# Optimization experiments

Hardware: AMD Instinct MI355X
Metric: run time of the kernel (lower is better)

## Reference

```python
import jax, jax.numpy as jnp
import numpy as np

B, T = 2, 2048
D_MODEL = 1024
N_LAYERS = 2
VOCAB = 256
BLOCK = 2048
LOCAL = 128
STRIDE = 256
NHEAD = D_MODEL // 64  # 16
HEAD_DIM = D_MODEL // NHEAD  # 64
LN_EPS = 1e-5


def setup_inputs() -> dict:
    key = jax.random.key(0)
    ks = jax.random.split(key, 16)
    L, d = N_LAYERS, D_MODEL

    def g(k, shape, scale=0.02):
        return (jax.random.normal(k, shape, dtype=jnp.float32) * scale)

    return {
        "x": jax.random.randint(ks[0], (B, T), 0, VOCAB),
        "embed": g(ks[1], (VOCAB, d)),
        "pos_embed": g(ks[2], (BLOCK, d)),
        # per-layer weights stacked on leading L axis; Linear as y = x @ W + b
        "Wq": g(ks[3], (L, d, d)), "bq": jnp.zeros((L, d), jnp.float32),
        "Wk": g(ks[4], (L, d, d)), "bk": jnp.zeros((L, d), jnp.float32),
        "Wv": g(ks[5], (L, d, d)), "bv": jnp.zeros((L, d), jnp.float32),
        "Wo": g(ks[6], (L, d, d)), "bo": jnp.zeros((L, d), jnp.float32),
        "g1": jnp.ones((L, d), jnp.float32), "be1": jnp.zeros((L, d), jnp.float32),
        "W1": g(ks[7], (L, d, 4 * d)), "bf1": jnp.zeros((L, 4 * d), jnp.float32),
        "W2": g(ks[8], (L, 4 * d, d)), "bf2": jnp.zeros((L, d), jnp.float32),
        "g2": jnp.ones((L, d), jnp.float32), "be2": jnp.zeros((L, d), jnp.float32),
        "gf": jnp.ones((d,), jnp.float32), "bef": jnp.zeros((d,), jnp.float32),
        "Whead": g(ks[9], (d, VOCAB)),
    }


def _ln(x, gamma, beta):
    mu = jnp.mean(x, axis=-1, keepdims=True)
    var = jnp.mean(jnp.square(x - mu), axis=-1, keepdims=True)
    return (x - mu) * jax.lax.rsqrt(var + LN_EPS) * gamma + beta


def _sparse_mask(t):
    # allowed[i, j] = True if token i may attend to token j
    i = jnp.arange(t)[:, None]
    j = jnp.arange(t)[None, :]
    causal = j <= i
    local = (i - j) <= LOCAL
    glob = (j % STRIDE) == 0
    return causal & (local | glob)


def _sparse_attn(q, k, v, allowed):
    # q, k, v: [B, T, D] -> [B, H, T, hd]
    b, t, d = q.shape
    def split(x):
        return x.reshape(b, t, NHEAD, HEAD_DIM).transpose(0, 2, 1, 3)
    q, k, v = split(q), split(k), split(v)
    scale = HEAD_DIM ** -0.5
    scores = jnp.einsum("bhqd,bhkd->bhqk", q, k) * scale
    scores = jnp.where(allowed[None, None], scores, -jnp.inf)
    attn = jax.nn.softmax(scores, axis=-1)  # every row has j=i allowed -> no NaN
    out = jnp.einsum("bhqk,bhkd->bhqd", attn, v)
    return out.transpose(0, 2, 1, 3).reshape(b, t, d)


def reference(x, embed, pos_embed, Wq, bq, Wk, bk, Wv, bv, Wo, bo,
              g1, be1, W1, bf1, W2, bf2, g2, be2, gf, bef, Whead):
    b, t = x.shape
    h = embed[x] + pos_embed[jnp.arange(t)][None]
    allowed = _sparse_mask(t)
    for l in range(N_LAYERS):
        h_n = _ln(h, g1[l], be1[l])
        q = h_n @ Wq[l] + bq[l]
        k = h_n @ Wk[l] + bk[l]
        v = h_n @ Wv[l] + bv[l]
        attn_out = _sparse_attn(q, k, v, allowed)
        h = h + (attn_out @ Wo[l] + bo[l])
        h2 = _ln(h, g2[l], be2[l])
        ffn = jax.nn.gelu(h2 @ W1[l] + bf1[l], approximate=False) @ W2[l] + bf2[l]
        h = h + ffn
    h = _ln(h, gf, bef)
    return h @ Whead
```

## Files before the change

### kernel.cpp

```cpp
#include <hip/hip_runtime.h>
#include <hip/hip_bf16.h>

#define BB 2
#define TT 2048
#define DD 1024
#define FF 4096
#define VV 256
#define HH 16
#define HD 64
#define MM (BB * TT)
#define LOCAL_W 128
#define STRIDE_G 256
#define QS 3072

typedef short s16x8 __attribute__((ext_vector_type(8)));
typedef __bf16 bf16x8 __attribute__((ext_vector_type(8)));
typedef float f32x4 __attribute__((ext_vector_type(4)));

#define WAITVM(N) asm volatile("s_waitcnt vmcnt(" #N ")" ::: "memory")
#define LGKM0 do { asm volatile("s_waitcnt lgkmcnt(0)" ::: "memory"); \
                   __builtin_amdgcn_sched_barrier(0); } while (0)

__device__ __forceinline__ float b2f(unsigned short u) {
  return __builtin_bit_cast(float, (unsigned int)u << 16);
}
__device__ __forceinline__ unsigned short f2b(float f) {
  __hip_bfloat16 h = __float2bfloat16(f);
  return __builtin_bit_cast(unsigned short, h);
}
__device__ __forceinline__ void gl_lds16(const unsigned short* g, unsigned short* l) {
  __builtin_amdgcn_global_load_lds(
      (const __attribute__((address_space(1))) void*)g,
      (__attribute__((address_space(3))) void*)l, 16, 0, 0);
}
__device__ __forceinline__ bf16x8 ldsr(const unsigned short* p) {
  return __builtin_bit_cast(bf16x8, *(const s16x8*)p);
}

__global__ __launch_bounds__(256) void transpose_k(const float* __restrict__ W,
                                                   unsigned short* __restrict__ WT,
                                                   int K, int N) {
  __shared__ float t[32][33];
  const int n0 = blockIdx.x * 32, k0 = blockIdx.y * 32;
  const int tx = threadIdx.x, ty = threadIdx.y;
  for (int r = ty; r < 32; r += 8) t[r][tx] = W[(size_t)(k0 + r) * N + n0 + tx];
  __syncthreads();
  for (int r = ty; r < 32; r += 8)
    WT[(size_t)(n0 + r) * K + k0 + tx] = f2b(t[tx][r]);
}

__global__ __launch_bounds__(256) void concat_bias(const float* __restrict__ bq,
                                                   const float* __restrict__ bk,
                                                   const float* __restrict__ bv,
                                                   float* __restrict__ bcat) {
  const int i = blockIdx.x * 256 + threadIdx.x;
  const int l = i / QS, j = i - l * QS;
  float v;
  if (j < DD) v = bq[l * DD + j];
  else if (j < 2 * DD) v = bk[l * DD + j - DD];
  else v = bv[l * DD + j - 2 * DD];
  bcat[i] = v;
}

__global__ __launch_bounds__(256) void embed_kernel(const int* __restrict__ x,
                                                    const float* __restrict__ emb,
                                                    const float* __restrict__ pos,
                                                    float* __restrict__ h) {
  const int row = blockIdx.x;
  const int c = threadIdx.x * 4;
  const int tok = x[row];
  const int t = row & (TT - 1);
  float4 e = *(const float4*)&emb[(size_t)tok * DD + c];
  float4 p = *(const float4*)&pos[(size_t)t * DD + c];
  e.x += p.x; e.y += p.y; e.z += p.z; e.w += p.w;
  *(float4*)&h[(size_t)row * DD + c] = e;
}

__global__ __launch_bounds__(256) void ln_kernel(const float* __restrict__ x,
                                                 const float* __restrict__ g,
                                                 const float* __restrict__ be,
                                                 unsigned short* __restrict__ out) {
  const int row = blockIdx.x;
  const int tid = threadIdx.x;
  const float4 v = *(const float4*)&x[(size_t)row * DD + tid * 4];
  float s = v.x + v.y + v.z + v.w;
  float sq = v.x * v.x + v.y * v.y + v.z * v.z + v.w * v.w;
#pragma unroll
  for (int off = 32; off; off >>= 1) {
    s += __shfl_xor(s, off);
    sq += __shfl_xor(sq, off);
  }
  __shared__ float ss[4], ssq[4];
  const int w = tid >> 6, lane = tid & 63;
  if (lane == 0) { ss[w] = s; ssq[w] = sq; }
  __syncthreads();
  s = ss[0] + ss[1] + ss[2] + ss[3];
  sq = ssq[0] + ssq[1] + ssq[2] + ssq[3];
  const float mean = s * (1.0f / DD);
  const float var = sq * (1.0f / DD) - mean * mean;
  const float rstd = rsqrtf(var + 1e-5f);
  const float4 gv = *(const float4*)&g[tid * 4];
  const float4 bv = *(const float4*)&be[tid * 4];
  ushort4 o;
  o.x = f2b((v.x - mean) * rstd * gv.x + bv.x);
  o.y = f2b((v.y - mean) * rstd * gv.y + bv.y);
  o.z = f2b((v.z - mean) * rstd * gv.z + bv.z);
  o.w = f2b((v.w - mean) * rstd * gv.w + bv.w);
  *(ushort4*)&out[(size_t)row * DD + tid * 4] = o;
}

template <int EPI>
__global__ __launch_bounds__(512, 2) void gemm8p(const unsigned short* __restrict__ A,
                                                 const unsigned short* __restrict__ BT,
                                                 const float* __restrict__ bias,
                                                 unsigned short* __restrict__ outp,
                                                 int M, int N, int K, int nbx) {
  __shared__ __align__(16) unsigned short lds[65536];
  const int tid = threadIdx.x;
  const int lane = tid & 63;
  const int w = tid >> 6;
  const int nwg = gridDim.x;
  const int orig = blockIdx.x;
  const int wg = (orig & 7) * (nwg >> 3) + (orig >> 3);
  const int n0 = (wg % nbx) * 256, m0 = (wg / nbx) * 256;
  const int wm = w >> 2, wn = w & 3;
  f32x4 acc[8][4] = {};

  const unsigned short* aSrc[2];
  const unsigned short* bSrc[2];
  int dstO[2];
#pragma unroll
  for (int i = 0; i < 2; i++) {
    const int s = tid + (i << 9);
    const int row = s >> 2, sc = s & 3;
    const int l = sc ^ ((row >> 1) & 3);
    aSrc[i] = &A[(size_t)(m0 + row) * K + l * 8];
    bSrc[i] = &BT[(size_t)(n0 + row) * K + l * 8];
    dstO[i] = s * 8;
  }
  auto STAGE = [&](int tb, int ks, int obase) {
    const int kt = (tb << 6) + (ks << 5);
    const int so = obase + ks * 16384;
#pragma unroll
    for (int i = 0; i < 2; i++) {
      gl_lds16(aSrc[i] + kt, &lds[so + dstO[i]]);
      gl_lds16(bSrc[i] + kt, &lds[so + 8192 + dstO[i]]);
    }
  };

  const int rA = lane & 15, cr = lane >> 4;
  const int rowA0 = wm * 128 + rA;
  const int rowB0 = wn * 64 + rA;
  const int aAddr0 = rowA0 * 32 + ((cr ^ ((rowA0 >> 1) & 3)) << 3);
  const int bAddr0 = 8192 + rowB0 * 32 + ((cr ^ ((rowB0 >> 1) & 3)) << 3);

  const int NT = K >> 6;
  STAGE(0, 0, 0);
  STAGE(0, 1, 0);

  auto TILE = [&](int bufc, int tb, bool notlast) {
    const int bb = bufc << 15;
    const int ob = (bufc ^ 1) << 15;
    bf16x8 bfr[4], af[4];
    WAITVM(4);
    __builtin_amdgcn_s_barrier();
#pragma unroll
    for (int n = 0; n < 4; n++) bfr[n] = ldsr(&lds[bb + bAddr0 + n * 512]);
#pragma unroll
    for (int i = 0; i < 4; i++) af[i] = ldsr(&lds[bb + aAddr0 + i * 512]);
    if (notlast) STAGE(tb + 1, 0, ob);
    LGKM0;
    __builtin_amdgcn_s_setprio(1);
#pragma unroll
    for (int i = 0; i < 4; i++)
#pragma unroll
      for (int n = 0; n < 4; n++)
        acc[i][n] = __builtin_amdgcn_mfma_f32_16x16x32_bf16(af[i], bfr[n], acc[i][n], 0, 0, 0);
    __builtin_amdgcn_s_setprio(0);
#pragma unroll
    for (int i = 0; i < 4; i++) af[i] = ldsr(&lds[bb + aAddr0 + (4 + i) * 512]);
    LGKM0;
    __builtin_amdgcn_s_setprio(1);
#pragma unroll
    for (int i = 0; i < 4; i++)
#pragma unroll
      for (int n = 0; n < 4; n++)
        acc[4 + i][n] = __builtin_amdgcn_mfma_f32_16x16x32_bf16(af[i], bfr[n], acc[4 + i][n], 0, 0, 0);
    __builtin_amdgcn_s_setprio(0);
    if (notlast) { WAITVM(4); } else { WAITVM(0); }
    __builtin_amdgcn_s_barrier();
#pragma unroll
    for (int n = 0; n < 4; n++) bfr[n] = ldsr(&lds[bb + 16384 + bAddr0 + n * 512]);
#pragma unroll
    for (int i = 0; i < 4; i++) af[i] = ldsr(&lds[bb + 16384 + aAddr0 + i * 512]);
    if (notlast) STAGE(tb + 1, 1, ob);
    LGKM0;
    __builtin_amdgcn_s_setprio(1);
#pragma unroll
    for (int i = 0; i < 4; i++)
#pragma unroll
      for (int n = 0; n < 4; n++)
        acc[i][n] = __builtin_amdgcn_mfma_f32_16x16x32_bf16(af[i], bfr[n], acc[i][n], 0, 0, 0);
    __builtin_amdgcn_s_setprio(0);
#pragma unroll
    for (int i = 0; i < 4; i++) af[i] = ldsr(&lds[bb + 16384 + aAddr0 + (4 + i) * 512]);
    LGKM0;
    __builtin_amdgcn_s_setprio(1);
#pragma unroll
    for (int i = 0; i < 4; i++)
#pragma unroll
      for (int n = 0; n < 4; n++)
        acc[4 + i][n] = __builtin_amdgcn_mfma_f32_16x16x32_bf16(af[i], bfr[n], acc[4 + i][n], 0, 0, 0);
    __builtin_amdgcn_s_setprio(0);
  };

  for (int it = 0; it < NT; it += 2) {
    TILE(0, it, true);
    TILE(1, it + 1, it + 2 < NT);
  }

  const int r0 = (lane >> 4) * 4;
  const int cc = lane & 15;
#pragma unroll
  for (int m = 0; m < 8; m++) {
#pragma unroll
    for (int n = 0; n < 4; n++) {
#pragma unroll
      for (int r = 0; r < 4; r++) {
        const int row = m0 + wm * 128 + m * 16 + r0 + r;
        const int col = n0 + wn * 64 + n * 16 + cc;
        float val = acc[m][n][r] + bias[col];
        if (EPI == 3) {
          float u = val * (0.7978845608f + 0.0356774081f * val * val);
          u = fminf(u, 10.0f);
          const float e = __expf(2.0f * u);
          val = val * e / (e + 1.0f);
        }
        outp[(size_t)row * N + col] = f2b(val);
      }
    }
  }
}

template <int EPI>
__global__ __launch_bounds__(512, 2) void gemm_p(const unsigned short* __restrict__ A,
                                                 const unsigned short* __restrict__ BT,
                                                 const float* __restrict__ bias,
                                                 const float* __restrict__ res,
                                                 void* __restrict__ outp,
                                                 int M, int N, int K, int nbx, int nwg2,
                                                 int ksub) {
  constexpr int BM = 128;
  __shared__ __align__(16) unsigned short lds[4][BM * 64];
  const int tid = threadIdx.x;
  const int lane = tid & 63;
  const int w = tid >> 6;
  const int nwg = gridDim.x;
  const int orig = blockIdx.x;
  const int wg = (orig & 7) * (nwg >> 3) + (orig >> 3);
  const int ks = wg / nwg2;
  const int rem = wg - ks * nwg2;
  const int n0 = (rem % nbx) * BM;
  const int m0 = (rem / nbx) * BM;
  const int kb = ks * ksub;
  const int wm = w >> 2, wn = w & 3;
  f32x4 acc[4][2] = {};

  auto STAGE = [&](int t) {
    const int b = t & 3;
    const int kt = kb + (t << 5);
    const int s = tid;
    const int row = s >> 2, sc = s & 3;
    const int c = sc ^ ((row >> 1) & 3);
    gl_lds16(&A[(size_t)(m0 + row) * K + kt + c * 8], &lds[b][s * 8]);
    gl_lds16(&BT[(size_t)(n0 + row) * K + kt + c * 8], &lds[b][BM * 32 + s * 8]);
  };

  const int NT = ksub >> 5;
  STAGE(0); STAGE(1); STAGE(2);

  for (int t = 0; t < NT; ++t) {
    const int ahead = NT - 1 - t;
    if (ahead >= 2) WAITVM(4); else if (ahead == 1) WAITVM(2); else WAITVM(0);
    __builtin_amdgcn_s_barrier();
    asm volatile("" ::: "memory");
    if (t + 3 < NT) STAGE(t + 3);
    const int b = t & 3;
    const int rA = lane & 15, cr = lane >> 4;
    bf16x8 af[4], bfr[2];
#pragma unroll
    for (int m = 0; m < 4; m++) {
      const int row = wm * 64 + m * 16 + rA;
      af[m] = ldsr(&lds[b][row * 32 + ((cr ^ ((row >> 1) & 3)) << 3)]);
    }
#pragma unroll
    for (int n = 0; n < 2; n++) {
      const int row = wn * 32 + n * 16 + rA;
      bfr[n] = ldsr(&lds[b][BM * 32 + row * 32 + ((cr ^ ((row >> 1) & 3)) << 3)]);
    }
    __builtin_amdgcn_s_setprio(1);
#pragma unroll
    for (int m = 0; m < 4; m++)
#pragma unroll
      for (int n = 0; n < 2; n++)
        acc[m][n] = __builtin_amdgcn_mfma_f32_16x16x32_bf16(af[m], bfr[n], acc[m][n], 0, 0, 0);
    __builtin_amdgcn_s_setprio(0);
  }

  const int r0 = (lane >> 4) * 4;
  const int cc = lane & 15;
  float* pout = (EPI == 0) ? ((float*)outp + (size_t)ks * M * N) : (float*)outp;
#pragma unroll
  for (int m = 0; m < 4; m++) {
#pragma unroll
    for (int n = 0; n < 2; n++) {
#pragma unroll
      for (int r = 0; r < 4; r++) {
        const int row = m0 + wm * 64 + m * 16 + r0 + r;
        const int col = n0 + wn * 32 + n * 16 + cc;
        const size_t idx = (size_t)row * N + col;
        if (EPI == 0) {
          pout[idx] = acc[m][n][r];
        } else {
          ((float*)outp)[idx] = acc[m][n][r] + bias[col] + res[idx];
        }
      }
    }
  }
}

template <int NP, bool BIAS, bool RES>
__global__ __launch_bounds__(256) void reduce_k(float* __restrict__ dst,
                                                const float* __restrict__ parts,
                                                const float* __restrict__ bias,
                                                int ncols, size_t total) {
  const size_t i = ((size_t)blockIdx.x * 256 + threadIdx.x) * 4;
  if (i >= total) return;
  f32x4 acc = {};
  if (RES) acc = *(const f32x4*)&dst[i];
  if (BIAS) {
    const int col = (int)(i % ncols);
    acc += *(const f32x4*)&bias[col];
  }
#pragma unroll
  for (int p = 0; p < NP; p++) acc += *(const f32x4*)&parts[(size_t)p * total + i];
  *(f32x4*)&dst[i] = acc;
}

#define QT 16
#define KT 32
#define NTMAX 6
#define KP 72
#define PP 40

__global__ __launch_bounds__(256) void attn_mfma(const unsigned short* __restrict__ qkv,
                                                 unsigned short* __restrict__ outg) {
  __shared__ __align__(16) unsigned short kvs[4][KT * KP];
  __shared__ __align__(16) unsigned short pls[4][QT * PP];
  const int tid = threadIdx.x;
  const int wid = tid >> 6, lane = tid & 63;
  const int qgrp = blockIdx.x & 31;
  const int bh = blockIdx.x >> 5;
  const int h = bh & (HH - 1), b = bh >> 4;
  const size_t baseq = (size_t)b * TT * QS + (size_t)h * HD;
  const size_t baseo = (size_t)b * TT * DD + (size_t)h * HD;
  const int i0 = qgrp * 64 + wid * 16;
  const int g = lane >> 4;
  const int c = lane & 15;

  const int i0b = qgrp * 64 + 48;
  const int ka0b = (i0b > 128) ? ((i0b - 128) & ~31) : 0;
  const int nlb = ((i0b + 16 - ka0b) + 31) >> 5;
  const int neb = (ka0b + 255) >> 8;
  const int ka0 = (i0 > 128) ? ((i0 - 128) & ~31) : 0;
  const int ne = (ka0 + 255) >> 8;

  const s16x8 qf0 = *(const s16x8*)&qkv[baseq + (size_t)(i0 + c) * QS + g * 8];
  const s16x8 qf1 = *(const s16x8*)&qkv[baseq + (size_t)(i0 + c) * QS + 32 + g * 8];

  f32x4 sc[NTMAX][2];
  float smax[4] = {-1e30f, -1e30f, -1e30f, -1e30f};

#pragma unroll
  for (int t = 0; t < NTMAX; t++) {
    if (t > nlb) continue;
    const bool isg = (t == 0);
    if (isg && neb == 0) continue;
    const int kt0 = ka0 + (t - 1) * 32;
#pragma unroll
    for (int it = 0; it < 4; it++) {
      const int row = it * 8 + (lane >> 3);
      const int ch = lane & 7;
      const int j = isg ? ((row < ne) ? row * STRIDE_G : 0) : (kt0 + row);
      *(s16x8*)&kvs[wid][row * KP + ch * 8] =
          *(const s16x8*)&qkv[baseq + DD + (size_t)j * QS + ch * 8];
    }
    __syncthreads();
#pragma unroll
    for (int half = 0; half < 2; half++) {
      const int key = half * 16 + c;
      const bf16x8 kb0 = __builtin_bit_cast(bf16x8, *(const s16x8*)&kvs[wid][key * KP + g * 8]);
      const bf16x8 kb1 = __builtin_bit_cast(bf16x8, *(const s16x8*)&kvs[wid][key * KP + 32 + g * 8]);
      f32x4 a = {};
      a = __builtin_amdgcn_mfma_f32_16x16x32_bf16(__builtin_bit_cast(bf16x8, qf0), kb0, a, 0, 0, 0);
      a = __builtin_amdgcn_mfma_f32_16x16x32_bf16(__builtin_bit_cast(bf16x8, qf1), kb1, a, 0, 0, 0);
#pragma unroll
      for (int r = 0; r < 4; r++) {
        const int i = i0 + g * 4 + r;
        bool ok;
        if (isg) {
          ok = (key < ne);
        } else {
          const int j = kt0 + key;
          ok = (j <= i) && (((i - j) <= LOCAL_W) || ((j & (STRIDE_G - 1)) == 0));
        }
        const float s = ok ? a[r] * 0.125f : -1e30f;
        sc[t][half][r] = s;
        smax[r] = fmaxf(smax[r], s);
      }
    }
    __syncthreads();
  }
#pragma unroll
  for (int r = 0; r < 4; r++)
#pragma unroll
    for (int off = 8; off; off >>= 1)
      smax[r] = fmaxf(smax[r], __shfl_xor(smax[r], off));

  f32x4 o[4] = {};
  float lsum[4] = {0.f, 0.f, 0.f, 0.f};
#pragma unroll
  for (int t = 0; t < NTMAX; t++) {
    if (t > nlb) continue;
    const bool isg = (t == 0);
    if (isg && neb == 0) continue;
    const int kt0 = ka0 + (t - 1) * 32;
#pragma unroll
    for (int it = 0; it < 4; it++) {
      const int row = it * 8 + (lane >> 3);
      const int ch = lane & 7;
      const int j = isg ? ((row < ne) ? row * STRIDE_G : 0) : (kt0 + row);
      *(s16x8*)&kvs[wid][row * KP + ch * 8] =
          *(const s16x8*)&qkv[baseq + 2 * DD + (size_t)j * QS + ch * 8];
    }
#pragma unroll
    for (int half = 0; half < 2; half++)
#pragma unroll
      for (int r = 0; r < 4; r++) {
        const float p = __expf(sc[t][half][r] - smax[r]);
        lsum[r] += p;
        pls[wid][(g * 4 + r) * PP + half * 16 + c] = f2b(p);
      }
    __syncthreads();
    const bf16x8 pa = __builtin_bit_cast(bf16x8, *(const s16x8*)&pls[wid][c * PP + g * 8]);
#pragma unroll
    for (int d0 = 0; d0 < 4; d0++) {
      s16x8 bv;
#pragma unroll
      for (int e = 0; e < 8; e++)
        bv[e] = (short)kvs[wid][(g * 8 + e) * KP + d0 * 16 + c];
      o[d0] = __builtin_amdgcn_mfma_f32_16x16x32_bf16(pa, __builtin_bit_cast(bf16x8, bv), o[d0], 0, 0, 0);
    }
    __syncthreads();
  }
#pragma unroll
  for (int r = 0; r < 4; r++)
#pragma unroll
    for (int off = 8; off; off >>= 1)
      lsum[r] += __shfl_xor(lsum[r], off);
#pragma unroll
  for (int d0 = 0; d0 < 4; d0++)
#pragma unroll
    for (int r = 0; r < 4; r++)
      outg[baseo + (size_t)(i0 + g * 4 + r) * DD + d0 * 16 + c] = f2b(o[d0][r] / lsum[r]);
}

extern "C" void kernel_launch(void* const* d_in, const int* in_sizes, int n_in,
                              void* d_out, int out_size, void* d_ws, size_t ws_size,
                              hipStream_t stream) {
  const int* x = (const int*)d_in[0];
  const float* embed = (const float*)d_in[1];
  const float* pos = (const float*)d_in[2];
  const float* Wq = (const float*)d_in[3];
  const float* bq = (const float*)d_in[4];
  const float* Wk = (const float*)d_in[5];
  const float* bk = (const float*)d_in[6];
  const float* Wv = (const float*)d_in[7];
  const float* bv = (const float*)d_in[8];
  const float* Wo = (const float*)d_in[9];
  const float* bo = (const float*)d_in[10];
  const float* g1 = (const float*)d_in[11];
  const float* be1 = (const float*)d_in[12];
  const float* W1 = (const float*)d_in[13];
  const float* bf1 = (const float*)d_in[14];
  const float* W2 = (const float*)d_in[15];
  const float* bf2 = (const float*)d_in[16];
  const float* g2 = (const float*)d_in[17];
  const float* be2 = (const float*)d_in[18];
  const float* gf = (const float*)d_in[19];
  const float* bef = (const float*)d_in[20];
  const float* Whead = (const float*)d_in[21];

  char* ws = (char*)d_ws;
  size_t off = 0;
  auto alloc = [&](size_t bytes) -> void* {
    void* p = ws + off;
    off += (bytes + 255) & ~(size_t)255;
    return p;
  };
  unsigned short* WqkvT = (unsigned short*)alloc((size_t)2 * QS * DD * 2);
  unsigned short* WoT = (unsigned short*)alloc((size_t)2 * DD * DD * 2);
  unsigned short* W1T = (unsigned short*)alloc((size_t)2 * DD * FF * 2);
  unsigned short* W2T = (unsigned short*)alloc((size_t)2 * DD * FF * 2);
  unsigned short* WheadT = (unsigned short*)alloc((size_t)DD * VV * 2);
  float* bcat = (float*)alloc((size_t)2 * QS * 4);
  float* h = (float*)alloc((size_t)MM * DD * 4);
  unsigned short* hn = (unsigned short*)alloc((size_t)MM * DD * 2);
  unsigned short* qkvb = (unsigned short*)alloc((size_t)MM * QS * 2);
  unsigned short* attnb = (unsigned short*)alloc((size_t)MM * DD * 2);
  unsigned short* mid = (unsigned short*)alloc((size_t)MM * FF * 2);
  float* ffn2p = (float*)qkvb;
  float* headp = (float*)mid;
  (void)ws_size;

  const dim3 tb(32, 8);
  for (int l = 0; l < 2; l++) {
    const size_t wo = (size_t)l * DD * DD;
    const size_t wf = (size_t)l * DD * FF;
    transpose_k<<<dim3(DD / 32, DD / 32), tb, 0, stream>>>(Wq + wo, WqkvT + (size_t)l * QS * DD, DD, DD);
    transpose_k<<<dim3(DD / 32, DD / 32), tb, 0, stream>>>(Wk + wo, WqkvT + ((size_t)l * QS + DD) * DD, DD, DD);
    transpose_k<<<dim3(DD / 32, DD / 32), tb, 0, stream>>>(Wv + wo, WqkvT + ((size_t)l * QS + 2 * DD) * DD, DD, DD);
    transpose_k<<<dim3(DD / 32, DD / 32), tb, 0, stream>>>(Wo + wo, WoT + wo, DD, DD);
    transpose_k<<<dim3(FF / 32, DD / 32), tb, 0, stream>>>(W1 + wf, W1T + wf, DD, FF);
    transpose_k<<<dim3(DD / 32, FF / 32), tb, 0, stream>>>(W2 + wf, W2T + wf, FF, DD);
  }
  transpose_k<<<dim3(VV / 32, DD / 32), tb, 0, stream>>>(Whead, WheadT, DD, VV);
  concat_bias<<<24, 256, 0, stream>>>(bq, bk, bv, bcat);

  embed_kernel<<<MM, 256, 0, stream>>>(x, embed, pos, h);

  for (int l = 0; l < 2; l++) {
    const size_t wo = (size_t)l * DD * DD;
    const size_t wf = (size_t)l * DD * FF;
    ln_kernel<<<MM, 256, 0, stream>>>(h, g1 + l * DD, be1 + l * DD, hn);
    gemm8p<1><<<(QS / 256) * (MM / 256), 512, 0, stream>>>(
        hn, WqkvT + (size_t)l * QS * DD, bcat + l * QS, qkvb, MM, QS, DD, QS / 256);
    attn_mfma<<<BB * HH * (TT / 64), 256, 0, stream>>>(qkvb, attnb);
    gemm_p<2><<<(DD / 128) * (MM / 128), 512, 0, stream>>>(
        attnb, WoT + wo, bo + l * DD, h, h,
        MM, DD, DD, DD / 128, (DD / 128) * (MM / 128), DD);
    ln_kernel<<<MM, 256, 0, stream>>>(h, g2 + l * DD, be2 + l * DD, hn);
    gemm8p<3><<<(FF / 256) * (MM / 256), 512, 0, stream>>>(
        hn, W1T + wf, bf1 + l * FF, mid, MM, FF, DD, FF / 256);
    gemm_p<0><<<2 * (DD / 128) * (MM / 128), 512, 0, stream>>>(
        mid, W2T + wf, nullptr, nullptr, ffn2p,
        MM, DD, FF, DD / 128, (DD / 128) * (MM / 128), FF / 2);
    reduce_k<2, true, true><<<(MM * DD) / 1024, 256, 0, stream>>>(
        h, ffn2p, bf2 + l * DD, DD, (size_t)MM * DD);
  }
  ln_kernel<<<MM, 256, 0, stream>>>(h, gf, bef, hn);
  gemm_p<0><<<4 * (VV / 128) * (MM / 128), 512, 0, stream>>>(
      hn, WheadT, nullptr, nullptr, headp,
      MM, VV, DD, VV / 128, (VV / 128) * (MM / 128), DD / 4);
  reduce_k<4, false, false><<<(MM * VV) / 1024, 256, 0, stream>>>(
      (float*)d_out, headp, nullptr, VV, (size_t)MM * VV);
}
```

Before: 455.9 us.

## Fuse FFN split-K reduction with next LayerNorm and add 256x128 W2 GEMM

Result: faster. 438.6 us (-3.8%).

```diff
diff --git a/kernel.cpp b/kernel.cpp
--- a/kernel.cpp
+++ b/kernel.cpp
@@ -109,6 +109,46 @@
   *(ushort4*)&out[(size_t)row * DD + tid * 4] = o;
 }
 
+__global__ __launch_bounds__(256) void ln_red(float* __restrict__ hio,
+                                              const float* __restrict__ parts,
+                                              const float* __restrict__ bias,
+                                              const float* __restrict__ g,
+                                              const float* __restrict__ be,
+                                              unsigned short* __restrict__ out) {
+  const int row = blockIdx.x;
+  const int tid = threadIdx.x;
+  const size_t base = (size_t)row * DD + tid * 4;
+  f32x4 v = *(const f32x4*)&hio[base];
+  v += *(const f32x4*)&bias[tid * 4];
+  v += *(const f32x4*)&parts[base];
+  v += *(const f32x4*)&parts[(size_t)MM * DD + base];
+  *(f32x4*)&hio[base] = v;
+  float s = v[0] + v[1] + v[2] + v[3];
+  float sq = v[0] * v[0] + v[1] * v[1] + v[2] * v[2] + v[3] * v[3];
+#pragma unroll
+  for (int off = 32; off; off >>= 1) {
+    s += __shfl_xor(s, off);
+    sq += __shfl_xor(sq, off);
+  }
+  __shared__ float ss[4], ssq[4];
+  const int w = tid >> 6, lane = tid & 63;
+  if (lane == 0) { ss[w] = s; ssq[w] = sq; }
+  __syncthreads();
+  s = ss[0] + ss[1] + ss[2] + ss[3];
+  sq = ssq[0] + ssq[1] + ssq[2] + ssq[3];
+  const float mean = s * (1.0f / DD);
+  const float var = sq * (1.0f / DD) - mean * mean;
+  const float rstd = rsqrtf(var + 1e-5f);
+  const float4 gv = *(const float4*)&g[tid * 4];
+  const float4 bv = *(const float4*)&be[tid * 4];
+  ushort4 o;
+  o.x = f2b((v[0] - mean) * rstd * gv.x + bv.x);
+  o.y = f2b((v[1] - mean) * rstd * gv.y + bv.y);
+  o.z = f2b((v[2] - mean) * rstd * gv.z + bv.z);
+  o.w = f2b((v[3] - mean) * rstd * gv.w + bv.w);
+  *(ushort4*)&out[(size_t)row * DD + tid * 4] = o;
+}
+
 template <int EPI>
 __global__ __launch_bounds__(512, 2) void gemm8p(const unsigned short* __restrict__ A,
                                                  const unsigned short* __restrict__ BT,
@@ -240,6 +280,137 @@
       }
     }
   }
+}
+
+__global__ __launch_bounds__(512, 2) void gemm_dw(const unsigned short* __restrict__ A,
+                                                  const unsigned short* __restrict__ BT,
+                                                  float* __restrict__ partial,
+                                                  int M, int N, int K, int nbx, int nwg2,
+                                                  int ksub) {
+  __shared__ __align__(16) unsigned short lds[49152];
+  const int tid = threadIdx.x;
+  const int lane = tid & 63;
+  const int w = tid >> 6;
+  const int nwg = gridDim.x;
+  const int orig = blockIdx.x;
+  const int wg = (orig & 7) * (nwg >> 3) + (orig >> 3);
+  const int ks = wg / nwg2;
+  const int rem = wg - ks * nwg2;
+  const int n0 = (rem % nbx) * 128;
+  const int m0 = (rem / nbx) * 256;
+  const int kb = ks * ksub;
+  const int wm = w >> 2, wn = w & 3;
+  f32x4 acc[8][2] = {};
+
+  const unsigned short* aSrc[2];
+  const unsigned short* bSrc;
+  int dstA[2], dstB;
+#pragma unroll
+  for (int i = 0; i < 2; i++) {
+    const int s = tid + (i << 9);
+    const int row = s >> 2, sc = s & 3;
+    const int l = sc ^ ((row >> 1) & 3);
+    aSrc[i] = &A[(size_t)(m0 + row) * K + kb + l * 8];
+    dstA[i] = s * 8;
+  }
+  {
+    const int row = tid >> 2, sc = tid & 3;
+    const int l = sc ^ ((row >> 1) & 3);
+    bSrc = &BT[(size_t)(n0 + row) * K + kb + l * 8];
+    dstB = 8192 + tid * 8;
+  }
+  auto STAGE = [&](int tb, int kss, int obase) {
+    const int kt = (tb << 6) + (kss << 5);
+    const int so = obase + kss * 12288;
+    gl_lds16(aSrc[0] + kt, &lds[so + dstA[0]]);
+    gl_lds16(aSrc[1] + kt, &lds[so + dstA[1]]);
+    gl_lds16(bSrc + kt, &lds[so + dstB]);
+  };
+
+  const int rA = lane & 15, cr = lane >> 4;
+  const int rowA0 = wm * 128 + rA;
+  const int rowB0 = wn * 32 + rA;
+  const int aAddr0 = rowA0 * 32 + ((cr ^ ((rowA0 >> 1) & 3)) << 3);
+  const int bAddr0 = 8192 + rowB0 * 32 + ((cr ^ ((rowB0 >> 1) & 3)) << 3);
+
+  const int NT = ksub >> 6;
+  STAGE(0, 0, 0);
+  STAGE(0, 1, 0);
+
+  auto TILE = [&](int bufc, int tb, bool notlast) {
+    const int bb = bufc * 24576;
+    const int ob = (bufc ^ 1) * 24576;
+    bf16x8 bfr[2], af[4];
+    WAITVM(3);
+    __builtin_amdgcn_s_barrier();
+#pragma unroll
+    for (int n = 0; n < 2; n++) bfr[n] = ldsr(&lds[bb + bAddr0 + n * 512]);
+#pragma unroll
+    for (int i = 0; i < 4; i++) af[i] = ldsr(&lds[bb + aAddr0 + i * 512]);
+    if (notlast) STAGE(tb + 1, 0, ob);
+    LGKM0;
+    __builtin_amdgcn_s_setprio(1);
+#pragma unroll
+    for (int i = 0; i < 4; i++)
+#pragma unroll
+      for (int n = 0; n < 2; n++)
+        acc[i][n] = __builtin_amdgcn_mfma_f32_16x16x32_bf16(af[i], bfr[n], acc[i][n], 0, 0, 0);
+    __builtin_amdgcn_s_setprio(0);
+#pragma unroll
+    for (int i = 0; i < 4; i++) af[i] = ldsr(&lds[bb + aAddr0 + (4 + i) * 512]);
+    LGKM0;
+    __builtin_amdgcn_s_setprio(1);
+#pragma unroll
+    for (int i = 0; i < 4; i++)
+#pragma unroll
+      for (int n = 0; n < 2; n++)
+        acc[4 + i][n] = __builtin_amdgcn_mfma_f32_16x16x32_bf16(af[i], bfr[n], acc[4 + i][n], 0, 0, 0);
+    __builtin_amdgcn_s_setprio(0);
+    if (notlast) { WAITVM(3); } else { WAITVM(0); }
+    __builtin_amdgcn_s_barrier();
+#pragma unroll
+    for (int n = 0; n < 2; n++) bfr[n] = ldsr(&lds[bb + 12288 + bAddr0 + n * 512]);
+#pragma unroll
+    for (int i = 0; i < 4; i++) af[i] = ldsr(&lds[bb + 12288 + aAddr0 + i * 512]);
+    if (notlast) STAGE(tb + 1, 1, ob);
+    LGKM0;
+    __builtin_amdgcn_s_setprio(1);
+#pragma unroll
+    for (int i = 0; i < 4; i++)
+#pragma unroll
+      for (int n = 0; n < 2; n++)
+        acc[i][n] = __builtin_amdgcn_mfma_f32_16x16x32_bf16(af[i], bfr[n], acc[i][n], 0, 0, 0);
+    __builtin_amdgcn_s_setprio(0);
+#pragma unroll
+    for (int i = 0; i < 4; i++) af[i] = ldsr(&lds[bb + 12288 + aAddr0 + (4 + i) * 512]);
+    LGKM0;
+    __builtin_amdgcn_s_setprio(1);
+#pragma unroll
+    for (int i = 0; i < 4; i++)
+#pragma unroll
+      for (int n = 0; n < 2; n++)
+        acc[4 + i][n] = __builtin_amdgcn_mfma_f32_16x16x32_bf16(af[i], bfr[n], acc[4 + i][n], 0, 0, 0);
+    __builtin_amdgcn_s_setprio(0);
+  };
+
+  for (int it = 0; it < NT; it += 2) {
+    TILE(0, it, true);
+    TILE(1, it + 1, it + 2 < NT);
+  }
+
+  float* pout = partial + (size_t)ks * M * N;
+  const int r0 = (lane >> 4) * 4;
+  const int cc = lane & 15;
+#pragma unroll
+  for (int m = 0; m < 8; m++)
+#pragma unroll
+    for (int n = 0; n < 2; n++)
+#pragma unroll
+      for (int r = 0; r < 4; r++) {
+        const int row = m0 + wm * 128 + m * 16 + r0 + r;
+        const int col = n0 + wn * 32 + n * 16 + cc;
+        pout[(size_t)row * N + col] = acc[m][n][r];
+      }
 }
 
 template <int EPI>
@@ -329,19 +500,13 @@
   }
 }
 
-template <int NP, bool BIAS, bool RES>
+template <int NP>
 __global__ __launch_bounds__(256) void reduce_k(float* __restrict__ dst,
                                                 const float* __restrict__ parts,
-                                                const float* __restrict__ bias,
-                                                int ncols, size_t total) {
+                                                size_t total) {
   const size_t i = ((size_t)blockIdx.x * 256 + threadIdx.x) * 4;
   if (i >= total) return;
   f32x4 acc = {};
-  if (RES) acc = *(const f32x4*)&dst[i];
-  if (BIAS) {
-    const int col = (int)(i % ncols);
-    acc += *(const f32x4*)&bias[col];
-  }
 #pragma unroll
   for (int p = 0; p < NP; p++) acc += *(const f32x4*)&parts[(size_t)p * total + i];
   *(f32x4*)&dst[i] = acc;
@@ -538,11 +703,11 @@
   concat_bias<<<24, 256, 0, stream>>>(bq, bk, bv, bcat);
 
   embed_kernel<<<MM, 256, 0, stream>>>(x, embed, pos, h);
+  ln_kernel<<<MM, 256, 0, stream>>>(h, g1, be1, hn);
 
   for (int l = 0; l < 2; l++) {
     const size_t wo = (size_t)l * DD * DD;
     const size_t wf = (size_t)l * DD * FF;
-    ln_kernel<<<MM, 256, 0, stream>>>(h, g1 + l * DD, be1 + l * DD, hn);
     gemm8p<1><<<(QS / 256) * (MM / 256), 512, 0, stream>>>(
         hn, WqkvT + (size_t)l * QS * DD, bcat + l * QS, qkvb, MM, QS, DD, QS / 256);
     attn_mfma<<<BB * HH * (TT / 64), 256, 0, stream>>>(qkvb, attnb);
@@ -552,16 +717,16 @@
     ln_kernel<<<MM, 256, 0, stream>>>(h, g2 + l * DD, be2 + l * DD, hn);
     gemm8p<3><<<(FF / 256) * (MM / 256), 512, 0, stream>>>(
         hn, W1T + wf, bf1 + l * FF, mid, MM, FF, DD, FF / 256);
-    gemm_p<0><<<2 * (DD / 128) * (MM / 128), 512, 0, stream>>>(
-        mid, W2T + wf, nullptr, nullptr, ffn2p,
-        MM, DD, FF, DD / 128, (DD / 128) * (MM / 128), FF / 2);
-    reduce_k<2, true, true><<<(MM * DD) / 1024, 256, 0, stream>>>(
-        h, ffn2p, bf2 + l * DD, DD, (size_t)MM * DD);
-  }
-  ln_kernel<<<MM, 256, 0, stream>>>(h, gf, bef, hn);
+    gemm_dw<<<2 * (DD / 128) * (MM / 256), 512, 0, stream>>>(
+        mid, W2T + wf, ffn2p, MM, DD, FF, DD / 128, (DD / 128) * (MM / 256), FF / 2);
+    if (l == 0)
+      ln_red<<<MM, 256, 0, stream>>>(h, ffn2p, bf2, g1 + DD, be1 + DD, hn);
+    else
+      ln_red<<<MM, 256, 0, stream>>>(h, ffn2p, bf2 + DD, gf, bef, hn);
+  }
   gemm_p<0><<<4 * (VV / 128) * (MM / 128), 512, 0, stream>>>(
       hn, WheadT, nullptr, nullptr, headp,
       MM, VV, DD, VV / 128, (VV / 128) * (MM / 128), DD / 4);
-  reduce_k<4, false, false><<<(MM * VV) / 1024, 256, 0, stream>>>(
-      (float*)d_out, headp, nullptr, VV, (size_t)MM * VV);
-}
+  reduce_k<4><<<(MM * VV) / 1024, 256, 0, stream>>>(
+      (float*)d_out, headp, (size_t)MM * VV);
+}
```

## Unify GEMMs with deeper LDS pipeline and fuse split-K reduction into LayerNorm

Applied to the files above, without the earlier changes.

New measurement: 594.0 us. 1.3x slower.

```diff
diff --git a/kernel.cpp b/kernel.cpp
--- a/kernel.cpp
+++ b/kernel.cpp
@@ -18,8 +18,6 @@
 typedef float f32x4 __attribute__((ext_vector_type(4)));
 
 #define WAITVM(N) asm volatile("s_waitcnt vmcnt(" #N ")" ::: "memory")
-#define LGKM0 do { asm volatile("s_waitcnt lgkmcnt(0)" ::: "memory"); \
-                   __builtin_amdgcn_sched_barrier(0); } while (0)
 
 __device__ __forceinline__ float b2f(unsigned short u) {
   return __builtin_bit_cast(float, (unsigned int)u << 16);
@@ -109,114 +107,179 @@
   *(ushort4*)&out[(size_t)row * DD + tid * 4] = o;
 }
 
-template <int EPI>
-__global__ __launch_bounds__(512, 2) void gemm8p(const unsigned short* __restrict__ A,
+__global__ __launch_bounds__(256) void ln_red(float* __restrict__ hio,
+                                              const float* __restrict__ parts,
+                                              const float* __restrict__ bias,
+                                              const float* __restrict__ g,
+                                              const float* __restrict__ be,
+                                              unsigned short* __restrict__ out) {
+  const int row = blockIdx.x;
+  const int tid = threadIdx.x;
+  const size_t base = (size_t)row * DD + tid * 4;
+  f32x4 v = *(const f32x4*)&hio[base];
+  v += *(const f32x4*)&bias[tid * 4];
+  v += *(const f32x4*)&parts[base];
+  v += *(const f32x4*)&parts[(size_t)MM * DD + base];
+  *(f32x4*)&hio[base] = v;
+  float s = v[0] + v[1] + v[2] + v[3];
+  float sq = v[0] * v[0] + v[1] * v[1] + v[2] * v[2] + v[3] * v[3];
+#pragma unroll
+  for (int off = 32; off; off >>= 1) {
+    s += __shfl_xor(s, off);
+    sq += __shfl_xor(sq, off);
+  }
+  __shared__ float ss[4], ssq[4];
+  const int w = tid >> 6, lane = tid & 63;
+  if (lane == 0) { ss[w] = s; ssq[w] = sq; }
+  __syncthreads();
+  s = ss[0] + ss[1] + ss[2] + ss[3];
+  sq = ssq[0] + ssq[1] + ssq[2] + ssq[3];
+  const float mean = s * (1.0f / DD);
+  const float var = sq * (1.0f / DD) - mean * mean;
+  const float rstd = rsqrtf(var + 1e-5f);
+  const float4 gv = *(const float4*)&g[tid * 4];
+  const float4 bv = *(const float4*)&be[tid * 4];
+  ushort4 o;
+  o.x = f2b((v[0] - mean) * rstd * gv.x + bv.x);
+  o.y = f2b((v[1] - mean) * rstd * gv.y + bv.y);
+  o.z = f2b((v[2] - mean) * rstd * gv.z + bv.z);
+  o.w = f2b((v[3] - mean) * rstd * gv.w + bv.w);
+  *(ushort4*)&out[(size_t)row * DD + tid * 4] = o;
+}
+
+template <int BN, int EPI>
+__global__ __launch_bounds__(512, 2) void gemm_u(const unsigned short* __restrict__ A,
                                                  const unsigned short* __restrict__ BT,
                                                  const float* __restrict__ bias,
-                                                 unsigned short* __restrict__ outp,
-                                                 int M, int N, int K, int nbx) {
-  __shared__ __align__(16) unsigned short lds[65536];
+                                                 void* __restrict__ outp,
+                                                 int M, int N, int K, int nbx, int nwg2,
+                                                 int ksub) {
+  constexpr int NF = BN / 64;
+  constexpr int SLOT_A = 256 * 32;
+  constexpr int SLOT_B = BN * 32;
+  constexpr int SLOT = SLOT_A + SLOT_B;
+  __shared__ __align__(16) unsigned short lds[4 * SLOT];
   const int tid = threadIdx.x;
   const int lane = tid & 63;
   const int w = tid >> 6;
   const int nwg = gridDim.x;
   const int orig = blockIdx.x;
   const int wg = (orig & 7) * (nwg >> 3) + (orig >> 3);
-  const int n0 = (wg % nbx) * 256, m0 = (wg / nbx) * 256;
+  const int ks = wg / nwg2;
+  const int rem = wg - ks * nwg2;
+  const int n0 = (rem % nbx) * BN;
+  const int m0 = (rem / nbx) * 256;
+  const int kb = ks * ksub;
   const int wm = w >> 2, wn = w & 3;
-  f32x4 acc[8][4] = {};
+  f32x4 acc[8][NF] = {};
 
   const unsigned short* aSrc[2];
-  const unsigned short* bSrc[2];
-  int dstO[2];
+  int dstA[2];
 #pragma unroll
   for (int i = 0; i < 2; i++) {
     const int s = tid + (i << 9);
     const int row = s >> 2, sc = s & 3;
     const int l = sc ^ ((row >> 1) & 3);
-    aSrc[i] = &A[(size_t)(m0 + row) * K + l * 8];
-    bSrc[i] = &BT[(size_t)(n0 + row) * K + l * 8];
-    dstO[i] = s * 8;
-  }
-  auto STAGE = [&](int tb, int ks, int obase) {
-    const int kt = (tb << 6) + (ks << 5);
-    const int so = obase + ks * 16384;
-#pragma unroll
-    for (int i = 0; i < 2; i++) {
-      gl_lds16(aSrc[i] + kt, &lds[so + dstO[i]]);
-      gl_lds16(bSrc[i] + kt, &lds[so + 8192 + dstO[i]]);
-    }
+    aSrc[i] = &A[(size_t)(m0 + row) * K + kb + l * 8];
+    dstA[i] = s * 8;
+  }
+  const unsigned short* bSrc[2];
+  int dstB[2];
+#pragma unroll
+  for (int i = 0; i < (BN == 256 ? 2 : 1); i++) {
+    const int s = tid + (i << 9);
+    const int row = s >> 2, sc = s & 3;
+    const int l = sc ^ ((row >> 1) & 3);
+    bSrc[i] = &BT[(size_t)(n0 + row) * K + kb + l * 8];
+    dstB[i] = SLOT_A + s * 8;
+  }
+  auto STAGE = [&](int tb, int kss) {
+    const int kt = (tb << 6) + (kss << 5);
+    const int so = ((tb & 1) * 2 + kss) * SLOT;
+    gl_lds16(aSrc[0] + kt, &lds[so + dstA[0]]);
+    gl_lds16(aSrc[1] + kt, &lds[so + dstA[1]]);
+    gl_lds16(bSrc[0] + kt, &lds[so + dstB[0]]);
+    if (BN == 256) gl_lds16(bSrc[1] + kt, &lds[so + dstB[1]]);
+  };
+  auto waitL = [&](bool steady) {
+    if (steady) { if (BN == 256) WAITVM(4); else WAITVM(3); }
+    else WAITVM(0);
   };
 
   const int rA = lane & 15, cr = lane >> 4;
   const int rowA0 = wm * 128 + rA;
-  const int rowB0 = wn * 64 + rA;
+  const int rowB0 = wn * (BN / 4) + rA;
   const int aAddr0 = rowA0 * 32 + ((cr ^ ((rowA0 >> 1) & 3)) << 3);
-  const int bAddr0 = 8192 + rowB0 * 32 + ((cr ^ ((rowB0 >> 1) & 3)) << 3);
-
-  const int NT = K >> 6;
-  STAGE(0, 0, 0);
-  STAGE(0, 1, 0);
-
-  auto TILE = [&](int bufc, int tb, bool notlast) {
-    const int bb = bufc << 15;
-    const int ob = (bufc ^ 1) << 15;
-    bf16x8 bfr[4], af[4];
-    WAITVM(4);
+  const int bAddr0 = SLOT_A + rowB0 * 32 + ((cr ^ ((rowB0 >> 1) & 3)) << 3);
+
+  const int NT = ksub >> 6;
+  bf16x8 a0[4], a1[4], bA[NF], bB[NF];
+
+  STAGE(0, 0); STAGE(0, 1); STAGE(1, 0);
+  if (BN == 256) WAITVM(8); else WAITVM(6);
+  __builtin_amdgcn_s_barrier();
+#pragma unroll
+  for (int m = 0; m < 4; m++) a0[m] = ldsr(&lds[aAddr0 + m * 512]);
+#pragma unroll
+  for (int n = 0; n < NF; n++) bA[n] = ldsr(&lds[bAddr0 + n * 512]);
+
+  auto TILE = [&](const int buf, const int t) {
+    const int bb = buf * 2 * SLOT;
+    const int nb = (buf ^ 1) * 2 * SLOT;
+    const bool nl1 = t + 1 < NT, nl2 = t + 2 < NT;
+    waitL(nl1);
     __builtin_amdgcn_s_barrier();
-#pragma unroll
-    for (int n = 0; n < 4; n++) bfr[n] = ldsr(&lds[bb + bAddr0 + n * 512]);
-#pragma unroll
-    for (int i = 0; i < 4; i++) af[i] = ldsr(&lds[bb + aAddr0 + i * 512]);
-    if (notlast) STAGE(tb + 1, 0, ob);
-    LGKM0;
+    if (nl1) STAGE(t + 1, 1);
+#pragma unroll
+    for (int m = 0; m < 4; m++) a1[m] = ldsr(&lds[bb + aAddr0 + (4 + m) * 512]);
     __builtin_amdgcn_s_setprio(1);
 #pragma unroll
     for (int i = 0; i < 4; i++)
 #pragma unroll
-      for (int n = 0; n < 4; n++)
-        acc[i][n] = __builtin_amdgcn_mfma_f32_16x16x32_bf16(af[i], bfr[n], acc[i][n], 0, 0, 0);
+      for (int n = 0; n < NF; n++)
+        acc[i][n] = __builtin_amdgcn_mfma_f32_16x16x32_bf16(a0[i], bA[n], acc[i][n], 0, 0, 0);
     __builtin_amdgcn_s_setprio(0);
 #pragma unroll
-    for (int i = 0; i < 4; i++) af[i] = ldsr(&lds[bb + aAddr0 + (4 + i) * 512]);
-    LGKM0;
+    for (int m = 0; m < 4; m++) a0[m] = ldsr(&lds[bb + SLOT + aAddr0 + m * 512]);
+#pragma unroll
+    for (int n = 0; n < NF; n++) bB[n] = ldsr(&lds[bb + SLOT + bAddr0 + n * 512]);
     __builtin_amdgcn_s_setprio(1);
 #pragma unroll
     for (int i = 0; i < 4; i++)
 #pragma unroll
-      for (int n = 0; n < 4; n++)
-        acc[4 + i][n] = __builtin_amdgcn_mfma_f32_16x16x32_bf16(af[i], bfr[n], acc[4 + i][n], 0, 0, 0);
+      for (int n = 0; n < NF; n++)
+        acc[4 + i][n] = __builtin_amdgcn_mfma_f32_16x16x32_bf16(a1[i], bA[n], acc[4 + i][n], 0, 0, 0);
     __builtin_amdgcn_s_setprio(0);
-    if (notlast) { WAITVM(4); } else { WAITVM(0); }
+    waitL(nl1);
     __builtin_amdgcn_s_barrier();
-#pragma unroll
-    for (int n = 0; n < 4; n++) bfr[n] = ldsr(&lds[bb + 16384 + bAddr0 + n * 512]);
-#pragma unroll
-    for (int i = 0; i < 4; i++) af[i] = ldsr(&lds[bb + 16384 + aAddr0 + i * 512]);
-    if (notlast) STAGE(tb + 1, 1, ob);
-    LGKM0;
+    if (nl2) STAGE(t + 2, 0);
+#pragma unroll
+    for (int m = 0; m < 4; m++) a1[m] = ldsr(&lds[bb + SLOT + aAddr0 + (4 + m) * 512]);
     __builtin_amdgcn_s_setprio(1);
 #pragma unroll
     for (int i = 0; i < 4; i++)
 #pragma unroll
-      for (int n = 0; n < 4; n++)
-        acc[i][n] = __builtin_amdgcn_mfma_f32_16x16x32_bf16(af[i], bfr[n], acc[i][n], 0, 0, 0);
+      for (int n = 0; n < NF; n++)
+        acc[i][n] = __builtin_amdgcn_mfma_f32_16x16x32_bf16(a0[i], bB[n], acc[i][n], 0, 0, 0);
     __builtin_amdgcn_s_setprio(0);
-#pragma unroll
-    for (int i = 0; i < 4; i++) af[i] = ldsr(&lds[bb + 16384 + aAddr0 + (4 + i) * 512]);
-    LGKM0;
+    if (nl1) {
+#pragma unroll
+      for (int m = 0; m < 4; m++) a0[m] = ldsr(&lds[nb + aAddr0 + m * 512]);
+#pragma unroll
+      for (int n = 0; n < NF; n++) bA[n] = ldsr(&lds[nb + bAddr0 + n * 512]);
+    }
     __builtin_amdgcn_s_setprio(1);
 #pragma unroll
     for (int i = 0; i < 4; i++)
 #pragma unroll
-      for (int n = 0; n < 4; n++)
-        acc[4 + i][n] = __builtin_amdgcn_mfma_f32_16x16x32_bf16(af[i], bfr[n], acc[4 + i][n], 0, 0, 0);
+      for (int n = 0; n < NF; n++)
+        acc[4 + i][n] = __builtin_amdgcn_mfma_f32_16x16x32_bf16(a1[i], bB[n], acc[4 + i][n], 0, 0, 0);
     __builtin_amdgcn_s_setprio(0);
   };
 
   for (int it = 0; it < NT; it += 2) {
-    TILE(0, it, true);
-    TILE(1, it + 1, it + 2 < NT);
+    TILE(0, it);
+    TILE(1, it + 1);
   }
 
   const int r0 = (lane >> 4) * 4;
@@ -224,30 +287,32 @@
 #pragma unroll
   for (int m = 0; m < 8; m++) {
 #pragma unroll
-    for (int n = 0; n < 4; n++) {
+    for (int n = 0; n < NF; n++) {
 #pragma unroll
       for (int r = 0; r < 4; r++) {
         const int row = m0 + wm * 128 + m * 16 + r0 + r;
-        const int col = n0 + wn * 64 + n * 16 + cc;
-        float val = acc[m][n][r] + bias[col];
-        if (EPI == 3) {
-          float u = val * (0.7978845608f + 0.0356774081f * val * val);
-          u = fminf(u, 10.0f);
-          const float e = __expf(2.0f * u);
-          val = val * e / (e + 1.0f);
+        const int col = n0 + wn * (BN / 4) + n * 16 + cc;
+        const size_t idx = (size_t)row * N + col;
+        if (EPI == 0) {
+          ((float*)outp)[(size_t)ks * M * N + idx] = acc[m][n][r];
+        } else {
+          float val = acc[m][n][r] + bias[col];
+          if (EPI == 3) {
+            float u = val * (0.7978845608f + 0.0356774081f * val * val);
+            u = fminf(u, 10.0f);
+            const float e = __expf(2.0f * u);
+            val = val * e / (e + 1.0f);
+          }
+          ((unsigned short*)outp)[idx] = f2b(val);
         }
-        outp[(size_t)row * N + col] = f2b(val);
       }
     }
   }
 }
 
-template <int EPI>
 __global__ __launch_bounds__(512, 2) void gemm_p(const unsigned short* __restrict__ A,
                                                  const unsigned short* __restrict__ BT,
-                                                 const float* __restrict__ bias,
-                                                 const float* __restrict__ res,
-                                                 void* __restrict__ outp,
+                                                 float* __restrict__ outp,
                                                  int M, int N, int K, int nbx, int nwg2,
                                                  int ksub) {
   constexpr int BM = 128;
@@ -309,39 +374,26 @@
 
   const int r0 = (lane >> 4) * 4;
   const int cc = lane & 15;
-  float* pout = (EPI == 0) ? ((float*)outp + (size_t)ks * M * N) : (float*)outp;
-#pragma unroll
-  for (int m = 0; m < 4; m++) {
-#pragma unroll
-    for (int n = 0; n < 2; n++) {
+  float* pout = outp + (size_t)ks * M * N;
+#pragma unroll
+  for (int m = 0; m < 4; m++)
+#pragma unroll
+    for (int n = 0; n < 2; n++)
 #pragma unroll
       for (int r = 0; r < 4; r++) {
         const int row = m0 + wm * 64 + m * 16 + r0 + r;
         const int col = n0 + wn * 32 + n * 16 + cc;
-        const size_t idx = (size_t)row * N + col;
-        if (EPI == 0) {
-          pout[idx] = acc[m][n][r];
-        } else {
-          ((float*)outp)[idx] = acc[m][n][r] + bias[col] + res[idx];
-        }
+        pout[(size_t)row * N + col] = acc[m][n][r];
       }
-    }
-  }
-}
-
-template <int NP, bool BIAS, bool RES>
+}
+
+template <int NP>
 __global__ __launch_bounds__(256) void reduce_k(float* __restrict__ dst,
                                                 const float* __restrict__ parts,
-                                                const float* __restrict__ bias,
-                                                int ncols, size_t total) {
+                                                size_t total) {
   const size_t i = ((size_t)blockIdx.x * 256 + threadIdx.x) * 4;
   if (i >= total) return;
   f32x4 acc = {};
-  if (RES) acc = *(const f32x4*)&dst[i];
-  if (BIAS) {
-    const int col = (int)(i % ncols);
-    acc += *(const f32x4*)&bias[col];
-  }
 #pragma unroll
   for (int p = 0; p < NP; p++) acc += *(const f32x4*)&parts[(size_t)p * total + i];
   *(f32x4*)&dst[i] = acc;
@@ -520,6 +572,7 @@
   unsigned short* attnb = (unsigned short*)alloc((size_t)MM * DD * 2);
   unsigned short* mid = (unsigned short*)alloc((size_t)MM * FF * 2);
   float* ffn2p = (float*)qkvb;
+  float* oprojp = (float*)mid;
   float* headp = (float*)mid;
   (void)ws_size;
 
@@ -538,30 +591,32 @@
   concat_bias<<<24, 256, 0, stream>>>(bq, bk, bv, bcat);
 
   embed_kernel<<<MM, 256, 0, stream>>>(x, embed, pos, h);
+  ln_kernel<<<MM, 256, 0, stream>>>(h, g1, be1, hn);
 
   for (int l = 0; l < 2; l++) {
     const size_t wo = (size_t)l * DD * DD;
     const size_t wf = (size_t)l * DD * FF;
-    ln_kernel<<<MM, 256, 0, stream>>>(h, g1 + l * DD, be1 + l * DD, hn);
-    gemm8p<1><<<(QS / 256) * (MM / 256), 512, 0, stream>>>(
-        hn, WqkvT + (size_t)l * QS * DD, bcat + l * QS, qkvb, MM, QS, DD, QS / 256);
+    gemm_u<256, 1><<<(QS / 256) * (MM / 256), 512, 0, stream>>>(
+        hn, WqkvT + (size_t)l * QS * DD, bcat + l * QS, qkvb,
+        MM, QS, DD, QS / 256, (QS / 256) * (MM / 256), DD);
     attn_mfma<<<BB * HH * (TT / 64), 256, 0, stream>>>(qkvb, attnb);
-    gemm_p<2><<<(DD / 128) * (MM / 128), 512, 0, stream>>>(
-        attnb, WoT + wo, bo + l * DD, h, h,
-        MM, DD, DD, DD / 128, (DD / 128) * (MM / 128), DD);
-    ln_kernel<<<MM, 256, 0, stream>>>(h, g2 + l * DD, be2 + l * DD, hn);
-    gemm8p<3><<<(FF / 256) * (MM / 256), 512, 0, stream>>>(
-        hn, W1T + wf, bf1 + l * FF, mid, MM, FF, DD, FF / 256);
-    gemm_p<0><<<2 * (DD / 128) * (MM / 128), 512, 0, stream>>>(
-        mid, W2T + wf, nullptr, nullptr, ffn2p,
-        MM, DD, FF, DD / 128, (DD / 128) * (MM / 128), FF / 2);
-    reduce_k<2, true, true><<<(MM * DD) / 1024, 256, 0, stream>>>(
-        h, ffn2p, bf2 + l * DD, DD, (size_t)MM * DD);
-  }
-  ln_kernel<<<MM, 256, 0, stream>>>(h, gf, bef, hn);
-  gemm_p<0><<<4 * (VV / 128) * (MM / 128), 512, 0, stream>>>(
-      hn, WheadT, nullptr, nullptr, headp,
-      MM, VV, DD, VV / 128, (VV / 128) * (MM / 128), DD / 4);
-  reduce_k<4, false, false><<<(MM * VV) / 1024, 256, 0, stream>>>(
-      (float*)d_out, headp, nullptr, VV, (size_t)MM * VV);
-}
+    gemm_u<128, 0><<<2 * (DD / 128) * (MM / 256), 512, 0, stream>>>(
+        attnb, WoT + wo, nullptr, oprojp,
+        MM, DD, DD, DD / 128, (DD / 128) * (MM / 256), DD / 2);
+    ln_red<<<MM, 256, 0, stream>>>(h, oprojp, bo + l * DD, g2 + l * DD, be2 + l * DD, hn);
+    gemm_u<256, 3><<<(FF / 256) * (MM / 256), 512, 0, stream>>>(
+        hn, W1T + wf, bf1 + l * FF, mid,
+        MM, FF, DD, FF / 256, (FF / 256) * (MM / 256), DD);
+    gemm_u<128, 0><<<2 * (DD / 128) * (MM / 256), 512, 0, stream>>>(
+        mid, W2T + wf, nullptr, ffn2p,
+        MM, DD, FF, DD / 128, (DD / 128) * (MM / 256), FF / 2);
+    if (l == 0)
+      ln_red<<<MM, 256, 0, stream>>>(h, ffn2p, bf2, g1 + DD, be1 + DD, hn);
+    else
+      ln_red<<<MM, 256, 0, stream>>>(h, ffn2p, bf2 + DD, gf, bef, hn);
+  }
+  gemm_p<<<4 * (VV / 128) * (MM / 128), 512, 0, stream>>>(
+      hn, WheadT, headp, MM, VV, DD, VV / 128, (VV / 128) * (MM / 128), DD / 4);
+  reduce_k<4><<<(MM * VV) / 1024, 256, 0, stream>>>(
+      (float*)d_out, headp, (size_t)MM * VV);
+}
```
